# Performance work log

Hardware: AMD Instinct MI355X
Metric: run time of the kernel (lower is better)

The kernel has to match this reference:

```python
import jax, jax.numpy as jnp
import numpy as np

INV_SQRT_4PI = 0.28209479177387814  # 1/sqrt(4*pi)

def sh_l(r, l):
    """Real spherical harmonics of unit vectors r [..., 3], e3nn order,
    'integral' normalization (e3nn o3.spherical_harmonics default)."""
    x, y, z = r[..., 0], r[..., 1], r[..., 2]
    if l == 0:
        return jnp.full(r.shape[:-1] + (1,), INV_SQRT_4PI, r.dtype)
    if l == 1:
        return 0.4886025119029199 * r  # sqrt(3/(4pi)) * (x, y, z)
    s15 = 3.872983346207417 * INV_SQRT_4PI   # sqrt(15)/sqrt(4pi)
    s5 = 2.23606797749979 * INV_SQRT_4PI     # sqrt(5)/sqrt(4pi)
    return jnp.stack([
        s15 * x * z,
        s15 * x * y,
        s5 * (y * y - 0.5 * (x * x + z * z)),
        s15 * y * z,
        0.5 * s15 * (z * z - x * x),
    ], axis=-1)

def layer_norm(x, g, b, eps=1e-5):
    mu = jnp.mean(x, axis=-1, keepdims=True)
    var = jnp.mean((x - mu) ** 2, axis=-1, keepdims=True)
    return (x - mu) * jax.lax.rsqrt(var + eps) * g + b

def setup_inputs() -> dict:
    key = jax.random.key(0)
    N, C, L = 1024, 128, 3  # nodes, sphere_channels, lmax+1
    ks = jax.random.split(key, 12)
    s = 0.02
    return {
        "x_emb": jax.random.normal(ks[0], (N, 9, C), jnp.float32),
        "pos": jax.random.normal(ks[1], (N, 3), jnp.float32) * 3.0,
        "q_w": jax.random.normal(ks[2], (C, C), jnp.float32) * s,
        "q_b": jnp.zeros((C,), jnp.float32),
        "k_w": jax.random.normal(ks[3], (C, C), jnp.float32) * s,
        "k_b": jnp.zeros((C,), jnp.float32),
        "v_w": jax.random.normal(ks[4], (L, C, C), jnp.float32) * s,
        "v_b0": jnp.zeros((C,), jnp.float32),
        "out_w": jax.random.normal(ks[5], (L, C, C), jnp.float32) * s,
        "ln_g": jnp.ones((L, C), jnp.float32),
        "ln_b": jnp.zeros((L, C), jnp.float32),
        "batch": jnp.sort(jax.random.randint(ks[6], (N,), 0, 16)).astype(jnp.int64),
    }

def reference(x_emb, pos, q_w, q_b, k_w, k_b, v_w, v_b0, out_w, ln_g, ln_b, batch):
    N, _, C = x_emb.shape
    H = 8
    D = C // H
    degs = (1, 3, 5)  # 2l+1 for l = 0, 1, 2

    # pairwise unit displacements  [N, N, 3]
    diff = pos[:, None, :] - pos[None, :, :]
    dist = jnp.maximum(jnp.linalg.norm(diff, axis=-1, keepdims=True), 1e-8)
    r_hat = diff / dist

    same = batch[:, None] == batch[None, :]           # [N, N]
    valid = same & ~jnp.eye(N, dtype=bool)

    # per-degree features: split x_emb[:, 9, C] into [1, 3, 5]
    feats = [x_emb[:, 0:1], x_emb[:, 1:4], x_emb[:, 4:9]]

    # HTR invariant pairwise score  [N, N, C]
    score = jnp.zeros((N, N, C), x_emb.dtype)
    for l, f in enumerate(feats):
        sh = sh_l(r_hat, l)                           # [N, N, 2l+1]
        score = score + jnp.einsum('imc,ijm->ijc', f, sh) / degs[l]
    score = score * valid[..., None].astype(score.dtype)

    q = (score.mean(axis=1) @ q_w.T + q_b).reshape(N, H, D)
    k = (score.mean(axis=0) @ k_w.T + k_b).reshape(N, H, D)

    attn = jnp.einsum('ihd,jhd->hij', q, k) * (D ** -0.5)
    attn = jnp.where(same[None], attn, -jnp.inf)
    attn = jnp.nan_to_num(jax.nn.softmax(attn, axis=-1))

    outs = []
    for l, f in enumerate(feats):
        m = degs[l]
        v = f @ v_w[l].T
        if l == 0:
            v = v + v_b0
        v = v.reshape(N, m, H, D)
        o = jnp.einsum('hij,jmhd->imhd', attn, v).reshape(N, m, C)
        o = o @ out_w[l].T
        outs.append(layer_norm(f + o, ln_g[l], ln_b[l]))
    return jnp.concatenate(outs, axis=1)
```

## Files before the change

kernel.cpp:

```cpp
#include <hip/hip_runtime.h>
#include <hip/hip_bf16.h>
#include <math.h>

#define NN 1024

typedef __attribute__((ext_vector_type(8))) short bf16x8;
typedef __attribute__((ext_vector_type(4))) float f32x4;

__device__ __forceinline__ float wave_sum(float v) {
#pragma unroll
  for (int off = 32; off > 0; off >>= 1) v += __shfl_down(v, off);
  return v;
}
__device__ __forceinline__ float wave_max(float v) {
#pragma unroll
  for (int off = 32; off > 0; off >>= 1) v = fmaxf(v, __shfl_down(v, off));
  return v;
}
__device__ __forceinline__ short f2bf(float x) {
  __hip_bfloat16 b = __float2bfloat16(x);
  return *(short*)&b;
}

#define SH_C0 0.28209479177387814f
#define SH_C1 0.4886025119029199f
#define SH_S15 1.0925484305920792f
#define SH_S5 0.6307831305050401f

__global__ __launch_bounds__(256) void htr_geom(
    const float* __restrict__ qw, const float* __restrict__ kw,
    const float* __restrict__ vw, const float* __restrict__ ow,
    const float* __restrict__ x_emb, const float* __restrict__ pos,
    const int* __restrict__ batch, short* __restrict__ wbf,
    short* __restrict__ x_bf, short* __restrict__ fT,
    short* __restrict__ Wsh, short* __restrict__ rowm_bf) {
  const int b = blockIdx.x;
  const int tid = threadIdx.x;
  __shared__ short tile[128][34];
  __shared__ float red[4][9];
  __shared__ float sm[9];

  if (b < 8) {
    const float* src;
    if (b == 0) src = qw;
    else if (b == 1) src = kw;
    else if (b < 5) src = vw + (b - 2) * 16384;
    else src = ow + (b - 5) * 16384;
    short* dst = wbf + b * 16384;
    for (int idx = tid; idx < 16384; idx += 256) dst[idx] = f2bf(src[idx]);
  } else if (b < 1160) {
    int base = (b - 8) * 1024 + tid * 4;
    float4 v = *(const float4*)(x_emb + base);
    *(short4*)(x_bf + base) = make_short4(f2bf(v.x), f2bf(v.y), f2bf(v.z), f2bf(v.w));
  } else if (b < 1448) {
    const int sub = b - 1160;
    const int i0 = (sub & 31) * 32;
    const int m = sub >> 5;
#pragma unroll
    for (int it = 0; it < 16; ++it) {
      int e = tid + it * 256;
      int r = e >> 7, c = e & 127;
      tile[c][r] = f2bf(x_emb[((i0 + r) * 9 + m) * 128 + c]);
    }
    __syncthreads();
#pragma unroll
    for (int it = 0; it < 8; ++it) {
      int idx = tid + it * 256;
      int c = idx >> 4, ii2 = idx & 15;
      *(short2*)(fT + c * 9216 + m * 1024 + i0 + ii2 * 2) =
          make_short2(tile[c][ii2 * 2], tile[c][ii2 * 2 + 1]);
    }
  } else if (b < 2472) {
    const int j = b - 1448;
    const float pjx = pos[j * 3 + 0], pjy = pos[j * 3 + 1], pjz = pos[j * 3 + 2];
    const int bj = batch[j];
    short* wrow = Wsh + j * 9216;
    for (int i = tid; i < 1024; i += 256) {
      float dx = pos[i * 3 + 0] - pjx;
      float dy = pos[i * 3 + 1] - pjy;
      float dz = pos[i * 3 + 2] - pjz;
      bool ok = (i != j) && (batch[i] == bj);
      float okf = ok ? 1.f : 0.f;
      float d2 = dx * dx + dy * dy + dz * dz;
      float inv = okf / fmaxf(sqrtf(d2), 1e-8f);
      float x = dx * inv, y = dy * inv, z = dz * inv;
      wrow[0 * 1024 + i] = f2bf(SH_C0 * okf);
      wrow[1 * 1024 + i] = f2bf((SH_C1 * (1.f / 3.f)) * x);
      wrow[2 * 1024 + i] = f2bf((SH_C1 * (1.f / 3.f)) * y);
      wrow[3 * 1024 + i] = f2bf((SH_C1 * (1.f / 3.f)) * z);
      wrow[4 * 1024 + i] = f2bf((SH_S15 * 0.2f) * x * z);
      wrow[5 * 1024 + i] = f2bf((SH_S15 * 0.2f) * x * y);
      wrow[6 * 1024 + i] = f2bf((SH_S5 * 0.2f) * (y * y - 0.5f * (x * x + z * z)));
      wrow[7 * 1024 + i] = f2bf((SH_S15 * 0.2f) * y * z);
      wrow[8 * 1024 + i] = f2bf((0.5f * SH_S15 * 0.2f) * (z * z - x * x));
    }
  } else {
    const int i = b - 2472;
    const float px = pos[i * 3 + 0], py = pos[i * 3 + 1], pz = pos[i * 3 + 2];
    const int bi = batch[i];
    float s[9];
#pragma unroll
    for (int m = 0; m < 9; ++m) s[m] = 0.f;
    for (int j = tid; j < NN; j += 256) {
      if (j == i) continue;
      if (batch[j] != bi) continue;
      float dx = px - pos[j * 3 + 0];
      float dy = py - pos[j * 3 + 1];
      float dz = pz - pos[j * 3 + 2];
      float d2 = dx * dx + dy * dy + dz * dz;
      float inv = 1.0f / fmaxf(sqrtf(d2), 1e-8f);
      float x = dx * inv, y = dy * inv, z = dz * inv;
      s[0] += 1.0f;
      s[1] += x; s[2] += y; s[3] += z;
      s[4] += x * z; s[5] += x * y;
      s[6] += y * y - 0.5f * (x * x + z * z);
      s[7] += y * z;
      s[8] += z * z - x * x;
    }
    const int wave = tid >> 6, lane = tid & 63;
#pragma unroll
    for (int m = 0; m < 9; ++m) {
      float v = wave_sum(s[m]);
      if (lane == 0) red[wave][m] = v;
    }
    __syncthreads();
    if (tid < 9) {
      float v = red[0][tid] + red[1][tid] + red[2][tid] + red[3][tid];
      float scl = SH_S15 * 0.2f;
      if (tid == 0) scl = SH_C0;
      else if (tid < 4) scl = SH_C1 * (1.f / 3.f);
      else if (tid == 6) scl = SH_S5 * 0.2f;
      else if (tid == 8) scl = 0.5f * SH_S15 * 0.2f;
      sm[tid] = v * scl * (1.0f / 1024.0f);
    }
    __syncthreads();
    if (tid < 128) {
      float acc = 0.f;
#pragma unroll
      for (int m = 0; m < 9; ++m)
        acc = fmaf(sm[m], x_emb[(i * 9 + m) * 128 + tid], acc);
      rowm_bf[i * 128 + tid] = f2bf(acc);
    }
  }
}

#define CMS 16
__global__ __launch_bounds__(256) void htr_colmean_mfma(
    const short* __restrict__ Wsh, const short* __restrict__ fT,
    float* __restrict__ part) {
  const int jb = blockIdx.x * 64;
  const int ks = blockIdx.y;
  const int tid = threadIdx.x;
  const int w = tid >> 6, lane = tid & 63;
  const int q = lane >> 4, l15 = lane & 15;
  __shared__ short bt[32][584];

  const int j = jb + w * 16 + l15;
  const short* ap = Wsh + j * 9216 + ks * 576 + q * 8;
  bf16x8 A[18];
#pragma unroll
  for (int s = 0; s < 18; ++s) A[s] = *(const bf16x8*)(ap + s * 32);

  f32x4 acc[8];
#pragma unroll
  for (int t = 0; t < 8; ++t) acc[t] = (f32x4){0.f, 0.f, 0.f, 0.f};

  for (int tc = 0; tc < 4; ++tc) {
    __syncthreads();
#pragma unroll
    for (int it = 0; it < 9; ++it) {
      int idx = tid + it * 256;
      int c = idx / 72;
      int g = idx - c * 72;
      *(bf16x8*)(&bt[c][g * 8]) =
          *(const bf16x8*)(fT + (tc * 32 + c) * 9216 + ks * 576 + g * 8);
    }
    __syncthreads();
#pragma unroll
    for (int tl = 0; tl < 2; ++tl) {
      const int t = tc * 2 + tl;
      const short* brow = &bt[tl * 16 + l15][q * 8];
#pragma unroll
      for (int s = 0; s < 18; ++s) {
        bf16x8 b = *(const bf16x8*)(brow + s * 32);
        acc[t] = __builtin_amdgcn_mfma_f32_16x16x32_bf16(A[s], b, acc[t], 0, 0, 0);
      }
    }
  }
#pragma unroll
  for (int t = 0; t < 8; ++t)
#pragma unroll
    for (int r = 0; r < 4; ++r)
      part[(ks * 1024 + jb + w * 16 + q * 4 + r) * 128 + t * 16 + l15] =
          acc[t][r];
}

__global__ __launch_bounds__(64) void htr_proj(
    const short* __restrict__ rowm_bf, const float* __restrict__ part,
    const short* __restrict__ x_bf, const short* __restrict__ wbf,
    const float* __restrict__ q_b, const float* __restrict__ k_b,
    const float* __restrict__ v_b0, float* __restrict__ qbuf,
    float* __restrict__ khbuf, short* __restrict__ vbT) {
  const int ibase = blockIdx.x * 16;
  const int y = blockIdx.y;
  const int lane = threadIdx.x;
  const int q = lane >> 4, l15 = lane & 15;

  bf16x8 a[4];
  const short* bp;
  if (y == 0) {
    const short* ap = rowm_bf + (ibase + l15) * 128 + q * 8;
#pragma unroll
    for (int ks = 0; ks < 4; ++ks) a[ks] = *(const bf16x8*)(ap + ks * 32);
    bp = wbf + l15 * 128 + q * 8;
  } else if (y == 1) {
    const float* pp = part + (size_t)(ibase + l15) * 128;
#pragma unroll
    for (int ks = 0; ks < 4; ++ks) {
      float s0 = 0.f, s1 = 0.f, s2 = 0.f, s3 = 0.f;
      float s4 = 0.f, s5 = 0.f, s6 = 0.f, s7 = 0.f;
#pragma unroll
      for (int s = 0; s < CMS; ++s) {
        const float* ps = pp + s * 131072 + ks * 32 + q * 8;
        float4 u0 = *(const float4*)(ps);
        float4 u1 = *(const float4*)(ps + 4);
        s0 += u0.x; s1 += u0.y; s2 += u0.z; s3 += u0.w;
        s4 += u1.x; s5 += u1.y; s6 += u1.z; s7 += u1.w;
      }
      const float sc = 1.0f / 1024.0f;
      bf16x8 av;
      av[0] = f2bf(s0 * sc); av[1] = f2bf(s1 * sc);
      av[2] = f2bf(s2 * sc); av[3] = f2bf(s3 * sc);
      av[4] = f2bf(s4 * sc); av[5] = f2bf(s5 * sc);
      av[6] = f2bf(s6 * sc); av[7] = f2bf(s7 * sc);
      a[ks] = av;
    }
    bp = wbf + 16384 + l15 * 128 + q * 8;
  } else {
    const int m = y - 2;
    const int l = (m == 0) ? 0 : ((m < 4) ? 1 : 2);
    const short* ap = x_bf + ((ibase + l15) * 9 + m) * 128 + q * 8;
#pragma unroll
    for (int ks = 0; ks < 4; ++ks) a[ks] = *(const bf16x8*)(ap + ks * 32);
    bp = wbf + (2 + l) * 16384 + l15 * 128 + q * 8;
  }

  f32x4 acc[8];
#pragma unroll
  for (int t = 0; t < 8; ++t) {
    acc[t] = (f32x4){0.f, 0.f, 0.f, 0.f};
    const short* bt = bp + t * 2048;
#pragma unroll
    for (int ks = 0; ks < 4; ++ks) {
      bf16x8 b = *(const bf16x8*)(bt + ks * 32);
      acc[t] = __builtin_amdgcn_mfma_f32_16x16x32_bf16(a[ks], b, acc[t], 0, 0, 0);
    }
  }

  if (y == 0) {
#pragma unroll
    for (int t = 0; t < 8; ++t) {
      float bo = q_b[t * 16 + l15];
#pragma unroll
      for (int r = 0; r < 4; ++r)
        qbuf[(ibase + q * 4 + r) * 128 + t * 16 + l15] = acc[t][r] + bo;
    }
  } else if (y == 1) {
#pragma unroll
    for (int t = 0; t < 8; ++t) {
      float bo = k_b[t * 16 + l15];
#pragma unroll
      for (int r = 0; r < 4; ++r)
        khbuf[(t * 1024 + ibase + q * 4 + r) * 16 + l15] = acc[t][r] + bo;
    }
  } else {
    const int m = y - 2;
#pragma unroll
    for (int t = 0; t < 8; ++t) {
      float bias = (m == 0) ? v_b0[t * 16 + l15] : 0.f;
#pragma unroll
      for (int r = 0; r < 4; ++r)
        vbT[(t * 144 + m * 16 + l15) * 1024 + ibase + q * 4 + r] =
            f2bf(acc[t][r] + bias);
    }
  }
}

template <int NT0, int NT>
__device__ __forceinline__ void apply_phase(
    const short* P, const short* __restrict__ vbT,
    short* __restrict__ obuf_bf, int ibase, int h, int lane) {
  const int q = lane >> 4, l15 = lane & 15;
  const int xs = (l15 & 7) << 3;
  const short* pr = P + l15 * 1024;
  const short* bp = vbT + (h * 144 + l15) * 1024 + q * 8;
  f32x4 acc[NT];
#pragma unroll
  for (int t = 0; t < NT; ++t) acc[t] = (f32x4){0.f, 0.f, 0.f, 0.f};
  bf16x8 a = *(const bf16x8*)(pr + ((q * 8) ^ xs));
  bf16x8 b[NT];
#pragma unroll
  for (int t = 0; t < NT; ++t) b[t] = *(const bf16x8*)(bp + (NT0 + t) * 16384);
  for (int ks = 1; ks < 32; ++ks) {
    const int off = ks * 32;
    bf16x8 an = *(const bf16x8*)(pr + ((off + q * 8) ^ xs));
    bf16x8 bn[NT];
#pragma unroll
    for (int t = 0; t < NT; ++t)
      bn[t] = *(const bf16x8*)(bp + (NT0 + t) * 16384 + off);
#pragma unroll
    for (int t = 0; t < NT; ++t)
      acc[t] = __builtin_amdgcn_mfma_f32_16x16x32_bf16(a, b[t], acc[t], 0, 0, 0);
    a = an;
#pragma unroll
    for (int t = 0; t < NT; ++t) b[t] = bn[t];
  }
#pragma unroll
  for (int t = 0; t < NT; ++t)
    acc[t] = __builtin_amdgcn_mfma_f32_16x16x32_bf16(a, b[t], acc[t], 0, 0, 0);
#pragma unroll
  for (int t = 0; t < NT; ++t)
#pragma unroll
    for (int r = 0; r < 4; ++r)
      obuf_bf[((ibase + q * 4 + r) * 9 + NT0 + t) * 128 + h * 16 + l15] =
          f2bf(acc[t][r]);
}

__global__ __launch_bounds__(256) void htr_attn_apply(
    const float* __restrict__ qbuf, const float* __restrict__ khbuf,
    const int* __restrict__ batch, const short* __restrict__ vbT,
    short* __restrict__ obuf_bf) {
  const int ibase = blockIdx.x * 16;
  const int h = blockIdx.y;
  const int tid = threadIdx.x;
  const int w = tid >> 6;
  const int lane = tid & 63;
  __shared__ short P[16 * 1024];

  const int r0 = ibase + w * 4;
  float qr[4][16];
  int bi[4];
#pragma unroll
  for (int r = 0; r < 4; ++r) {
    bi[r] = batch[r0 + r];
    const float* qp = qbuf + (r0 + r) * 128 + h * 16;
#pragma unroll
    for (int d = 0; d < 16; ++d) qr[r][d] = qp[d] * 0.25f;
  }
  float s[4][16];
#pragma unroll
  for (int jt = 0; jt < 16; ++jt) {
    const int j = jt * 64 + lane;
    const int bj = batch[j];
    const float4* kp = (const float4*)(khbuf + (h * 1024 + j) * 16);
    float4 k0 = kp[0], k1 = kp[1], k2 = kp[2], k3 = kp[3];
#pragma unroll
    for (int r = 0; r < 4; ++r) {
      float d = 0.f;
      d = fmaf(qr[r][0], k0.x, d);  d = fmaf(qr[r][1], k0.y, d);
      d = fmaf(qr[r][2], k0.z, d);  d = fmaf(qr[r][3], k0.w, d);
      d = fmaf(qr[r][4], k1.x, d);  d = fmaf(qr[r][5], k1.y, d);
      d = fmaf(qr[r][6], k1.z, d);  d = fmaf(qr[r][7], k1.w, d);
      d = fmaf(qr[r][8], k2.x, d);  d = fmaf(qr[r][9], k2.y, d);
      d = fmaf(qr[r][10], k2.z, d); d = fmaf(qr[r][11], k2.w, d);
      d = fmaf(qr[r][12], k3.x, d); d = fmaf(qr[r][13], k3.y, d);
      d = fmaf(qr[r][14], k3.z, d); d = fmaf(qr[r][15], k3.w, d);
      s[r][jt] = (bj == bi[r]) ? d : -INFINITY;
    }
  }
#pragma unroll
  for (int r = 0; r < 4; ++r) {
    float mx = s[r][0];
#pragma unroll
    for (int jt = 1; jt < 16; ++jt) mx = fmaxf(mx, s[r][jt]);
    mx = wave_max(mx);
    mx = __shfl(mx, 0);
    float t = 0.f;
#pragma unroll
    for (int jt = 0; jt < 16; ++jt) {
      s[r][jt] = expf(s[r][jt] - mx);
      t += s[r][jt];
    }
    t = wave_sum(t);
    t = __shfl(t, 0);
    const float inv = 1.0f / t;
    const int row = w * 4 + r;
    const int xs = (row & 7) << 3;
    short* pw = P + row * 1024;
#pragma unroll
    for (int jt = 0; jt < 16; ++jt) {
      const int j = jt * 64 + lane;
      pw[j ^ xs] = f2bf(s[r][jt] * inv);
    }
  }
  __syncthreads();

  if (w == 0)      apply_phase<0, 3>(P, vbT, obuf_bf, ibase, h, lane);
  else if (w == 1) apply_phase<3, 2>(P, vbT, obuf_bf, ibase, h, lane);
  else if (w == 2) apply_phase<5, 2>(P, vbT, obuf_bf, ibase, h, lane);
  else             apply_phase<7, 2>(P, vbT, obuf_bf, ibase, h, lane);
}

__global__ __launch_bounds__(64) void htr_outln_mfma(
    const short* __restrict__ obuf_bf, const float* __restrict__ x_emb,
    const short* __restrict__ wbf, const float* __restrict__ ln_g,
    const float* __restrict__ ln_b, float* __restrict__ out) {
  const int ibase = blockIdx.x * 16;
  const int m = blockIdx.y;
  const int l = (m == 0) ? 0 : ((m < 4) ? 1 : 2);
  const int lane = threadIdx.x;
  const int q = lane >> 4, l15 = lane & 15;
  const short* ap = obuf_bf + ((ibase + l15) * 9 + m) * 128 + q * 8;
  const short* bp = wbf + (5 + l) * 16384 + l15 * 128 + q * 8;
  bf16x8 a[4];
#pragma unroll
  for (int ks = 0; ks < 4; ++ks) a[ks] = *(const bf16x8*)(ap + ks * 32);
  f32x4 acc[8];
#pragma unroll
  for (int t = 0; t < 8; ++t) {
    acc[t] = (f32x4){0.f, 0.f, 0.f, 0.f};
    const short* bt = bp + t * 2048;
#pragma unroll
    for (int ks = 0; ks < 4; ++ks) {
      bf16x8 b = *(const bf16x8*)(bt + ks * 32);
      acc[t] = __builtin_amdgcn_mfma_f32_16x16x32_bf16(a[ks], b, acc[t], 0, 0, 0);
    }
  }
  float g[8], bb[8];
#pragma unroll
  for (int t = 0; t < 8; ++t) {
    g[t] = ln_g[l * 128 + t * 16 + l15];
    bb[t] = ln_b[l * 128 + t * 16 + l15];
  }
#pragma unroll
  for (int r = 0; r < 4; ++r) {
    const int i = ibase + q * 4 + r;
    const float* xr = x_emb + (i * 9 + m) * 128;
    float v[8];
    float sv = 0.f, sq = 0.f;
#pragma unroll
    for (int t = 0; t < 8; ++t) {
      v[t] = acc[t][r] + xr[t * 16 + l15];
      sv += v[t];
      sq += v[t] * v[t];
    }
#pragma unroll
    for (int off = 1; off < 16; off <<= 1) {
      sv += __shfl_xor(sv, off);
      sq += __shfl_xor(sq, off);
    }
    float mu = sv * (1.f / 128.f);
    float var = sq * (1.f / 128.f) - mu * mu;
    float rs = rsqrtf(var + 1e-5f);
    float* orow = out + (i * 9 + m) * 128;
#pragma unroll
    for (int t = 0; t < 8; ++t)
      orow[t * 16 + l15] = (v[t] - mu) * rs * g[t] + bb[t];
  }
}

extern "C" void kernel_launch(void* const* d_in, const int* in_sizes, int n_in,
                              void* d_out, int out_size, void* d_ws, size_t ws_size,
                              hipStream_t stream) {
  (void)in_sizes; (void)n_in; (void)out_size; (void)ws_size;
  const float* x_emb = (const float*)d_in[0];
  const float* pos   = (const float*)d_in[1];
  const float* q_w   = (const float*)d_in[2];
  const float* q_b   = (const float*)d_in[3];
  const float* k_w   = (const float*)d_in[4];
  const float* k_b   = (const float*)d_in[5];
  const float* v_w   = (const float*)d_in[6];
  const float* v_b0  = (const float*)d_in[7];
  const float* out_w = (const float*)d_in[8];
  const float* ln_g  = (const float*)d_in[9];
  const float* ln_b  = (const float*)d_in[10];
  const int*   batch = (const int*)d_in[11];
  float* out = (float*)d_out;

  float* ws = (float*)d_ws;
  short* rowm_bf = (short*)(ws + 0);
  float* qbuf    = ws + 65536;
  float* khbuf   = ws + 196608;
  short* wbf     = (short*)(ws + 327680);
  short* x_bf    = (short*)(ws + 393216);
  short* vbT     = (short*)(ws + 983040);
  short* obuf_bf = (short*)(ws + 1572864);
  float* part    = ws + 2162688;
  short* Wsh     = (short*)(ws + 6356992);
  short* fT      = (short*)(ws + 11075584);

  htr_geom<<<3496, 256, 0, stream>>>(q_w, k_w, v_w, out_w, x_emb, pos, batch,
                                     wbf, x_bf, fT, Wsh, rowm_bf);
  htr_colmean_mfma<<<dim3(16, CMS), 256, 0, stream>>>(Wsh, fT, part);
  htr_proj<<<dim3(64, 11), 64, 0, stream>>>(rowm_bf, part, x_bf, wbf, q_b, k_b,
                                            v_b0, qbuf, khbuf, vbT);
  htr_attn_apply<<<dim3(64, 8), 256, 0, stream>>>(qbuf, khbuf, batch, vbT,
                                                  obuf_bf);
  htr_outln_mfma<<<dim3(64, 9), 64, 0, stream>>>(obuf_bf, x_emb, wbf, ln_g,
                                                 ln_b, out);
}
```

Before: 152.7 us.

## Fold K projection into feature transpose and merge colmean with projection kernel

The key weight is applied to the per-node features before the column-mean GEMM (linearity), so the colmean MFMA writes head-layout K directly via atomicAdd into a bias-initialised khbuf. This removes the partial-sum buffer, its 16-way reduction and the separate K projection. The colmean, Q projection and V projection are merged into one launch, so one kernel launch goes away. The costs are float atomics (nondeterministic summation order), an extra bf16 rounding of the projected features, and uncached fp32 weight loads in the transpose blocks.

```diff
diff --git a/kernel.cpp b/kernel.cpp
--- a/kernel.cpp
+++ b/kernel.cpp
@@ -31,12 +31,13 @@
     const float* __restrict__ qw, const float* __restrict__ kw,
     const float* __restrict__ vw, const float* __restrict__ ow,
     const float* __restrict__ x_emb, const float* __restrict__ pos,
-    const int* __restrict__ batch, short* __restrict__ wbf,
-    short* __restrict__ x_bf, short* __restrict__ fT,
-    short* __restrict__ Wsh, short* __restrict__ rowm_bf) {
+    const int* __restrict__ batch, const float* __restrict__ k_b,
+    short* __restrict__ wbf, short* __restrict__ x_bf,
+    short* __restrict__ fkT, short* __restrict__ Wsh,
+    short* __restrict__ rowm_bf, float* __restrict__ khbuf) {
   const int b = blockIdx.x;
   const int tid = threadIdx.x;
-  __shared__ short tile[128][34];
+  __shared__ short tile[128][36];
   __shared__ float red[4][9];
   __shared__ float sm[9];
 
@@ -56,20 +57,40 @@
     const int sub = b - 1160;
     const int i0 = (sub & 31) * 32;
     const int m = sub >> 5;
-#pragma unroll
-    for (int it = 0; it < 16; ++it) {
-      int e = tid + it * 256;
-      int r = e >> 7, c = e & 127;
-      tile[c][r] = f2bf(x_emb[((i0 + r) * 9 + m) * 128 + c]);
+    const int w = tid >> 6, lane = tid & 63;
+    const int q = lane >> 4, l15 = lane & 15;
+    const int isub = (w & 1) * 16;
+    const int cbase = (w >> 1) * 64;
+    bf16x8 a[4];
+#pragma unroll
+    for (int ks = 0; ks < 4; ++ks) {
+      const float* ap = x_emb + ((i0 + isub + l15) * 9 + m) * 128 + ks * 32 + q * 8;
+      bf16x8 av;
+#pragma unroll
+      for (int e = 0; e < 8; ++e) av[e] = f2bf(ap[e]);
+      a[ks] = av;
+    }
+#pragma unroll
+    for (int t = 0; t < 4; ++t) {
+      f32x4 acc = (f32x4){0.f, 0.f, 0.f, 0.f};
+#pragma unroll
+      for (int ks = 0; ks < 4; ++ks) {
+        const float* bp = kw + (cbase + t * 16 + l15) * 128 + ks * 32 + q * 8;
+        bf16x8 bv;
+#pragma unroll
+        for (int e = 0; e < 8; ++e) bv[e] = f2bf(bp[e]);
+        acc = __builtin_amdgcn_mfma_f32_16x16x32_bf16(a[ks], bv, acc, 0, 0, 0);
+      }
+#pragma unroll
+      for (int r = 0; r < 4; ++r)
+        tile[cbase + t * 16 + l15][isub + q * 4 + r] = f2bf(acc[r]);
     }
     __syncthreads();
-#pragma unroll
-    for (int it = 0; it < 8; ++it) {
-      int idx = tid + it * 256;
-      int c = idx >> 4, ii2 = idx & 15;
-      *(short2*)(fT + c * 9216 + m * 1024 + i0 + ii2 * 2) =
-          make_short2(tile[c][ii2 * 2], tile[c][ii2 * 2 + 1]);
-    }
+    const int cc = tid >> 1, seg = tid & 1;
+    short* dst = fkT + cc * 9216 + m * 1024 + i0 + seg * 16;
+#pragma unroll
+    for (int e = 0; e < 16; e += 2)
+      *(short2*)(dst + e) = *(const short2*)(&tile[cc][seg * 16 + e]);
   } else if (b < 2472) {
     const int j = b - 1448;
     const float pjx = pos[j * 3 + 0], pjy = pos[j * 3 + 1], pjz = pos[j * 3 + 2];
@@ -94,7 +115,7 @@
       wrow[7 * 1024 + i] = f2bf((SH_S15 * 0.2f) * y * z);
       wrow[8 * 1024 + i] = f2bf((0.5f * SH_S15 * 0.2f) * (z * z - x * x));
     }
-  } else {
+  } else if (b < 3496) {
     const int i = b - 2472;
     const float px = pos[i * 3 + 0], py = pos[i * 3 + 1], pz = pos[i * 3 + 2];
     const int bi = batch[i];
@@ -141,140 +162,114 @@
         acc = fmaf(sm[m], x_emb[(i * 9 + m) * 128 + tid], acc);
       rowm_bf[i * 128 + tid] = f2bf(acc);
     }
-  }
-}
-
-#define CMS 16
-__global__ __launch_bounds__(256) void htr_colmean_mfma(
-    const short* __restrict__ Wsh, const short* __restrict__ fT,
-    float* __restrict__ part) {
-  const int jb = blockIdx.x * 64;
-  const int ks = blockIdx.y;
+  } else {
+    const int base = (b - 3496) * 32768;
+    for (int u = tid; u < 32768; u += 256) {
+      const int idx = base + u;
+      khbuf[idx] = k_b[((idx >> 14) << 4) | (idx & 15)];
+    }
+  }
+}
+
+__global__ __launch_bounds__(256) void htr_mid(
+    const short* __restrict__ Wsh, const short* __restrict__ fkT,
+    const short* __restrict__ rowm_bf, const short* __restrict__ x_bf,
+    const short* __restrict__ wbf, const float* __restrict__ q_b,
+    const float* __restrict__ v_b0, float* __restrict__ khbuf,
+    float* __restrict__ qbuf, short* __restrict__ vbT) {
+  const int b = blockIdx.x;
   const int tid = threadIdx.x;
   const int w = tid >> 6, lane = tid & 63;
   const int q = lane >> 4, l15 = lane & 15;
   __shared__ short bt[32][584];
 
-  const int j = jb + w * 16 + l15;
-  const short* ap = Wsh + j * 9216 + ks * 576 + q * 8;
-  bf16x8 A[18];
-#pragma unroll
-  for (int s = 0; s < 18; ++s) A[s] = *(const bf16x8*)(ap + s * 32);
-
-  f32x4 acc[8];
-#pragma unroll
-  for (int t = 0; t < 8; ++t) acc[t] = (f32x4){0.f, 0.f, 0.f, 0.f};
-
-  for (int tc = 0; tc < 4; ++tc) {
-    __syncthreads();
-#pragma unroll
-    for (int it = 0; it < 9; ++it) {
-      int idx = tid + it * 256;
-      int c = idx / 72;
-      int g = idx - c * 72;
-      *(bf16x8*)(&bt[c][g * 8]) =
-          *(const bf16x8*)(fT + (tc * 32 + c) * 9216 + ks * 576 + g * 8);
-    }
-    __syncthreads();
-#pragma unroll
-    for (int tl = 0; tl < 2; ++tl) {
-      const int t = tc * 2 + tl;
-      const short* brow = &bt[tl * 16 + l15][q * 8];
-#pragma unroll
-      for (int s = 0; s < 18; ++s) {
-        bf16x8 b = *(const bf16x8*)(brow + s * 32);
-        acc[t] = __builtin_amdgcn_mfma_f32_16x16x32_bf16(A[s], b, acc[t], 0, 0, 0);
+  if (b < 256) {
+    const int jb = (b & 15) * 64;
+    const int ks = b >> 4;
+    const int j = jb + w * 16 + l15;
+    const short* ap = Wsh + j * 9216 + ks * 576 + q * 8;
+    bf16x8 A[18];
+#pragma unroll
+    for (int s = 0; s < 18; ++s) A[s] = *(const bf16x8*)(ap + s * 32);
+
+    f32x4 acc[8];
+#pragma unroll
+    for (int t = 0; t < 8; ++t) acc[t] = (f32x4){0.f, 0.f, 0.f, 0.f};
+
+    for (int tc = 0; tc < 4; ++tc) {
+      __syncthreads();
+#pragma unroll
+      for (int it = 0; it < 9; ++it) {
+        int idx = tid + it * 256;
+        int c = idx / 72;
+        int g = idx - c * 72;
+        *(bf16x8*)(&bt[c][g * 8]) =
+            *(const bf16x8*)(fkT + (tc * 32 + c) * 9216 + ks * 576 + g * 8);
       }
-    }
-  }
-#pragma unroll
-  for (int t = 0; t < 8; ++t)
-#pragma unroll
-    for (int r = 0; r < 4; ++r)
-      part[(ks * 1024 + jb + w * 16 + q * 4 + r) * 128 + t * 16 + l15] =
-          acc[t][r];
-}
-
-__global__ __launch_bounds__(64) void htr_proj(
-    const short* __restrict__ rowm_bf, const float* __restrict__ part,
-    const short* __restrict__ x_bf, const short* __restrict__ wbf,
-    const float* __restrict__ q_b, const float* __restrict__ k_b,
-    const float* __restrict__ v_b0, float* __restrict__ qbuf,
-    float* __restrict__ khbuf, short* __restrict__ vbT) {
-  const int ibase = blockIdx.x * 16;
-  const int y = blockIdx.y;
-  const int lane = threadIdx.x;
-  const int q = lane >> 4, l15 = lane & 15;
-
-  bf16x8 a[4];
-  const short* bp;
-  if (y == 0) {
+      __syncthreads();
+#pragma unroll
+      for (int tl = 0; tl < 2; ++tl) {
+        const int t = tc * 2 + tl;
+        const short* brow = &bt[tl * 16 + l15][q * 8];
+#pragma unroll
+        for (int s = 0; s < 18; ++s) {
+          bf16x8 bv = *(const bf16x8*)(brow + s * 32);
+          acc[t] = __builtin_amdgcn_mfma_f32_16x16x32_bf16(A[s], bv, acc[t], 0, 0, 0);
+        }
+      }
+    }
+#pragma unroll
+    for (int t = 0; t < 8; ++t)
+#pragma unroll
+      for (int r = 0; r < 4; ++r)
+        atomicAdd(&khbuf[(t * 1024 + jb + w * 16 + q * 4 + r) * 16 + l15],
+                  acc[t][r] * (1.0f / 1024.0f));
+  } else if (b < 272) {
+    const int ibase = ((b - 256) * 4 + w) * 16;
     const short* ap = rowm_bf + (ibase + l15) * 128 + q * 8;
+    const short* bp = wbf + l15 * 128 + q * 8;
+    bf16x8 a[4];
 #pragma unroll
     for (int ks = 0; ks < 4; ++ks) a[ks] = *(const bf16x8*)(ap + ks * 32);
-    bp = wbf + l15 * 128 + q * 8;
-  } else if (y == 1) {
-    const float* pp = part + (size_t)(ibase + l15) * 128;
-#pragma unroll
-    for (int ks = 0; ks < 4; ++ks) {
-      float s0 = 0.f, s1 = 0.f, s2 = 0.f, s3 = 0.f;
-      float s4 = 0.f, s5 = 0.f, s6 = 0.f, s7 = 0.f;
-#pragma unroll
-      for (int s = 0; s < CMS; ++s) {
-        const float* ps = pp + s * 131072 + ks * 32 + q * 8;
-        float4 u0 = *(const float4*)(ps);
-        float4 u1 = *(const float4*)(ps + 4);
-        s0 += u0.x; s1 += u0.y; s2 += u0.z; s3 += u0.w;
-        s4 += u1.x; s5 += u1.y; s6 += u1.z; s7 += u1.w;
+    f32x4 acc[8];
+#pragma unroll
+    for (int t = 0; t < 8; ++t) {
+      acc[t] = (f32x4){0.f, 0.f, 0.f, 0.f};
+      const short* btp = bp + t * 2048;
+#pragma unroll
+      for (int ks = 0; ks < 4; ++ks) {
+        bf16x8 bv = *(const bf16x8*)(btp + ks * 32);
+        acc[t] = __builtin_amdgcn_mfma_f32_16x16x32_bf16(a[ks], bv, acc[t], 0, 0, 0);
       }
-      const float sc = 1.0f / 1024.0f;
-      bf16x8 av;
-      av[0] = f2bf(s0 * sc); av[1] = f2bf(s1 * sc);
-      av[2] = f2bf(s2 * sc); av[3] = f2bf(s3 * sc);
-      av[4] = f2bf(s4 * sc); av[5] = f2bf(s5 * sc);
-      av[6] = f2bf(s6 * sc); av[7] = f2bf(s7 * sc);
-      a[ks] = av;
-    }
-    bp = wbf + 16384 + l15 * 128 + q * 8;
+    }
+#pragma unroll
+    for (int t = 0; t < 8; ++t) {
+      float bo = q_b[t * 16 + l15];
+#pragma unroll
+      for (int r = 0; r < 4; ++r)
+        qbuf[(ibase + q * 4 + r) * 128 + t * 16 + l15] = acc[t][r] + bo;
+    }
   } else {
-    const int m = y - 2;
+    const int u = (b - 272) * 4 + w;
+    const int m = u >> 6;
+    const int ibase = (u & 63) * 16;
     const int l = (m == 0) ? 0 : ((m < 4) ? 1 : 2);
     const short* ap = x_bf + ((ibase + l15) * 9 + m) * 128 + q * 8;
+    const short* bp = wbf + (2 + l) * 16384 + l15 * 128 + q * 8;
+    bf16x8 a[4];
 #pragma unroll
     for (int ks = 0; ks < 4; ++ks) a[ks] = *(const bf16x8*)(ap + ks * 32);
-    bp = wbf + (2 + l) * 16384 + l15 * 128 + q * 8;
-  }
-
-  f32x4 acc[8];
-#pragma unroll
-  for (int t = 0; t < 8; ++t) {
-    acc[t] = (f32x4){0.f, 0.f, 0.f, 0.f};
-    const short* bt = bp + t * 2048;
-#pragma unroll
-    for (int ks = 0; ks < 4; ++ks) {
-      bf16x8 b = *(const bf16x8*)(bt + ks * 32);
-      acc[t] = __builtin_amdgcn_mfma_f32_16x16x32_bf16(a[ks], b, acc[t], 0, 0, 0);
-    }
-  }
-
-  if (y == 0) {
+    f32x4 acc[8];
 #pragma unroll
     for (int t = 0; t < 8; ++t) {
-      float bo = q_b[t * 16 + l15];
-#pragma unroll
-      for (int r = 0; r < 4; ++r)
-        qbuf[(ibase + q * 4 + r) * 128 + t * 16 + l15] = acc[t][r] + bo;
-    }
-  } else if (y == 1) {
-#pragma unroll
-    for (int t = 0; t < 8; ++t) {
-      float bo = k_b[t * 16 + l15];
-#pragma unroll
-      for (int r = 0; r < 4; ++r)
-        khbuf[(t * 1024 + ibase + q * 4 + r) * 16 + l15] = acc[t][r] + bo;
-    }
-  } else {
-    const int m = y - 2;
+      acc[t] = (f32x4){0.f, 0.f, 0.f, 0.f};
+      const short* btp = bp + t * 2048;
+#pragma unroll
+      for (int ks = 0; ks < 4; ++ks) {
+        bf16x8 bv = *(const bf16x8*)(btp + ks * 32);
+        acc[t] = __builtin_amdgcn_mfma_f32_16x16x32_bf16(a[ks], bv, acc[t], 0, 0, 0);
+      }
+    }
 #pragma unroll
     for (int t = 0; t < 8; ++t) {
       float bias = (m == 0) ? v_b0[t * 16 + l15] : 0.f;
@@ -485,15 +480,13 @@
   short* x_bf    = (short*)(ws + 393216);
   short* vbT     = (short*)(ws + 983040);
   short* obuf_bf = (short*)(ws + 1572864);
-  float* part    = ws + 2162688;
   short* Wsh     = (short*)(ws + 6356992);
-  short* fT      = (short*)(ws + 11075584);
-
-  htr_geom<<<3496, 256, 0, stream>>>(q_w, k_w, v_w, out_w, x_emb, pos, batch,
-                                     wbf, x_bf, fT, Wsh, rowm_bf);
-  htr_colmean_mfma<<<dim3(16, CMS), 256, 0, stream>>>(Wsh, fT, part);
-  htr_proj<<<dim3(64, 11), 64, 0, stream>>>(rowm_bf, part, x_bf, wbf, q_b, k_b,
-                                            v_b0, qbuf, khbuf, vbT);
+  short* fkT     = (short*)(ws + 11075584);
+
+  htr_geom<<<3500, 256, 0, stream>>>(q_w, k_w, v_w, out_w, x_emb, pos, batch,
+                                     k_b, wbf, x_bf, fkT, Wsh, rowm_bf, khbuf);
+  htr_mid<<<416, 256, 0, stream>>>(Wsh, fkT, rowm_bf, x_bf, wbf, q_b, v_b0,
+                                   khbuf, qbuf, vbT);
   htr_attn_apply<<<dim3(64, 8), 256, 0, stream>>>(qbuf, khbuf, batch, vbT,
                                                   obuf_bf);
   htr_outln_mfma<<<dim3(64, 9), 64, 0, stream>>>(obuf_bf, x_emb, wbf, ln_g,
```

Result: no change. 152.6 us (-0.1%).
